# Performance work log

Measured on AMD Instinct MI355X. Metric: run time of the kernel, lower is better.

Reference implementation:

```python
import jax, jax.numpy as jnp
import numpy as np


def squash(v, axis=-1):
    # scale = |v|^2 / (1+|v|^2) / |v|  (exactly as in the source)
    s2 = jnp.sum(jnp.square(v), axis=axis, keepdims=True)
    scale = s2 / (1.0 + s2) / jnp.sqrt(s2)
    return scale * v


def setup_inputs() -> dict:
    key = jax.random.key(0)
    k1, k2 = jax.random.split(key)
    B, I, P = 64, 2048, 16   # batch, input_num_capsule, input_dim_vector
    J, D = 32, 32            # num_capsule, dim_vector
    inputs = jax.random.normal(k1, (B, I, P), dtype=jnp.float32)
    W = jax.random.normal(k2, (I, J, P, D), dtype=jnp.float32) * 0.1
    bias = jnp.zeros((1, I, J, 1, 1), dtype=jnp.float32)
    return {"inputs": inputs, "W": W, "bias": bias}


def reference(inputs, W, bias):
    # inputs_hat[b,i,j,d] = inputs[b,i,:] @ W[i,j,:,:]
    # (replaces the tf.scan over batch of per-capsule batch_dot)
    inputs_hat = jnp.einsum('bip,ijpd->bijd', inputs, W)

    # In the source while_loop, c = softmax(self.bias, dim=2) is computed from the
    # ORIGINAL bias every iteration (loop-carried b is never read), so all
    # num_routing iterations yield the identical output; compute it once.
    c = jax.nn.softmax(bias[:, :, :, 0, 0], axis=2)          # [1, I, J]
    s = jnp.einsum('bijd,xij->bjd', inputs_hat, c)            # sum over input capsules
    outputs = squash(s, axis=-1)                              # [B, J, D]
    return outputs
```

## Files before the change

### kernel.cpp

```cpp
#include <hip/hip_runtime.h>
#include <hip/hip_bf16.h>
#include <math.h>

#define I_CAP 2048
#define P_DIM 16
#define J_CAP 32
#define D_DIM 32
#define B_SZ  64
#define KCN   32
#define IPB   (I_CAP / KCN)
#define IPW   (IPB / 4)

typedef __attribute__((ext_vector_type(8)))  short short8_t;
typedef __attribute__((ext_vector_type(16))) float f32x16;

__device__ __forceinline__ short f2bf(float f) {
    __hip_bfloat16 h = __float2bfloat16(f);
    return __builtin_bit_cast(short, h);
}

__global__ __launch_bounds__(256, 2) void caps_main_k(const float* __restrict__ inputs,
                                                      const float* __restrict__ W,
                                                      const float* __restrict__ bias,
                                                      float* __restrict__ partial) {
    __shared__ float red[4 * 4096];
    __shared__ float c_lds[64][2];
    const int t  = threadIdx.x;
    const int l  = t & 63;
    const int wv = t >> 6;

    const int orig = blockIdx.x;
    const int wgid = (orig & 7) * 64 + (orig >> 3);
    const int kc = wgid >> 4;
    const int jp = wgid & 15;
    const int j0 = jp * 2;

    const int g  = l >> 5;
    const int dn = l & 31;

    const int i0blk = kc * IPB;
    const int i0    = i0blk + wv * IPW;

    {
        const int jj = t & 31;
        const int ib = t >> 5;
#pragma unroll
        for (int pass = 0; pass < 8; ++pass) {
            const int ii = pass * 8 + ib;
            float x = bias[(i0blk + ii) * J_CAP + jj];
            float m = x;
#pragma unroll
            for (int k = 16; k >= 1; k >>= 1) m = fmaxf(m, __shfl_xor(m, k));
            float e = expf(x - m);
            float s = e;
#pragma unroll
            for (int k = 16; k >= 1; k >>= 1) s += __shfl_xor(s, k);
            float cv = e / s;
            if (jj == j0)     c_lds[ii][0] = cv;
            if (jj == j0 + 1) c_lds[ii][1] = cv;
        }
    }
    __syncthreads();

    const float* wlane  = W + (((size_t)(i0 * J_CAP + j0)) << 9) + g * 256 + dn;
    const float* alane0 = inputs + ((size_t)dn << 15) + (size_t)i0 * 16 + g * 8;
    const float* alane1 = alane0 + ((size_t)32 << 15);

    f32x16 accA0 = {};
    f32x16 accA1 = {};
    f32x16 accB0 = {};
    f32x16 accB1 = {};

#pragma unroll 4
    for (int r = 0; r < IPW; ++r) {
        const float cj0 = c_lds[wv * IPW + r][0];
        const float cj1 = c_lds[wv * IPW + r][1];
        float w0buf[8], w1buf[8];
#pragma unroll
        for (int e = 0; e < 8; ++e) {
            w0buf[e] = wlane[(size_t)r * 16384 + e * 32];
            w1buf[e] = wlane[(size_t)r * 16384 + 512 + e * 32];
        }
        float4 a0 = *(const float4*)(alane0 + r * 16);
        float4 a1 = *(const float4*)(alane0 + r * 16 + 4);
        float4 a2 = *(const float4*)(alane1 + r * 16);
        float4 a3 = *(const float4*)(alane1 + r * 16 + 4);

        short8_t bf0, bf1, af0, af1;
#pragma unroll
        for (int e = 0; e < 8; ++e) bf0[e] = f2bf(w0buf[e] * cj0);
#pragma unroll
        for (int e = 0; e < 8; ++e) bf1[e] = f2bf(w1buf[e] * cj1);
        af0[0] = f2bf(a0.x); af0[1] = f2bf(a0.y); af0[2] = f2bf(a0.z); af0[3] = f2bf(a0.w);
        af0[4] = f2bf(a1.x); af0[5] = f2bf(a1.y); af0[6] = f2bf(a1.z); af0[7] = f2bf(a1.w);
        af1[0] = f2bf(a2.x); af1[1] = f2bf(a2.y); af1[2] = f2bf(a2.z); af1[3] = f2bf(a2.w);
        af1[4] = f2bf(a3.x); af1[5] = f2bf(a3.y); af1[6] = f2bf(a3.z); af1[7] = f2bf(a3.w);

        accA0 = __builtin_amdgcn_mfma_f32_32x32x16_bf16(af0, bf0, accA0, 0, 0, 0);
        accA1 = __builtin_amdgcn_mfma_f32_32x32x16_bf16(af1, bf0, accA1, 0, 0, 0);
        accB0 = __builtin_amdgcn_mfma_f32_32x32x16_bf16(af0, bf1, accB0, 0, 0, 0);
        accB1 = __builtin_amdgcn_mfma_f32_32x32x16_bf16(af1, bf1, accB1, 0, 0, 0);
    }

    {
        float* rw = red + wv * 4096;
#pragma unroll
        for (int reg = 0; reg < 16; ++reg) {
            const int b0 = (reg & 3) + 8 * (reg >> 2) + 4 * g;
            rw[b0 * 32 + dn]               = accA0[reg];
            rw[(b0 + 32) * 32 + dn]        = accA1[reg];
            rw[2048 + b0 * 32 + dn]        = accB0[reg];
            rw[2048 + (b0 + 32) * 32 + dn] = accB1[reg];
        }
    }
    __syncthreads();
    {
        float* dstbase = partial + (size_t)(kc * J_CAP + j0) * 2048;
#pragma unroll
        for (int jj = 0; jj < 2; ++jj) {
#pragma unroll
            for (int s = 0; s < 2; ++s) {
                const int o = jj * 2048 + s * 1024 + t * 4;
                float4 v0 = *(const float4*)(red + o);
                float4 v1 = *(const float4*)(red + 4096 + o);
                float4 v2 = *(const float4*)(red + 8192 + o);
                float4 v3 = *(const float4*)(red + 12288 + o);
                float4 sum = {v0.x + v1.x + v2.x + v3.x,
                              v0.y + v1.y + v2.y + v3.y,
                              v0.z + v1.z + v2.z + v3.z,
                              v0.w + v1.w + v2.w + v3.w};
                *(float4*)(dstbase + o) = sum;
            }
        }
    }
}

__global__ __launch_bounds__(256) void caps_reduce_squash_k(const float* __restrict__ partial,
                                                            float* __restrict__ out) {
    const int tid2 = blockIdx.x * 256 + threadIdx.x;
    const int row  = tid2 >> 4;
    const int sub  = tid2 & 15;
    const int d4   = sub >> 1;
    const int half = sub & 1;
    const int j = row >> 6, b = row & 63;

    const float* src = partial + ((size_t)(half * 16) * J_CAP + j) * 2048 + b * 32 + d4 * 4;
    float4 v = {0.f, 0.f, 0.f, 0.f};
#pragma unroll
    for (int kc = 0; kc < 16; ++kc) {
        float4 p = *(const float4*)(src + (size_t)kc * J_CAP * 2048);
        v.x += p.x; v.y += p.y; v.z += p.z; v.w += p.w;
    }
    v.x += __shfl_xor(v.x, 1); v.y += __shfl_xor(v.y, 1);
    v.z += __shfl_xor(v.z, 1); v.w += __shfl_xor(v.w, 1);

    float sq = v.x * v.x + v.y * v.y + v.z * v.z + v.w * v.w;
#pragma unroll
    for (int m = 2; m <= 8; m <<= 1) sq += __shfl_xor(sq, m);
    float scale = sq / (1.0f + sq) / sqrtf(sq);
    if (half == 0) {
        float4 o = {v.x * scale, v.y * scale, v.z * scale, v.w * scale};
        *(float4*)(out + (size_t)b * (J_CAP * D_DIM) + j * D_DIM + d4 * 4) = o;
    }
}

extern "C" void kernel_launch(void* const* d_in, const int* in_sizes, int n_in,
                              void* d_out, int out_size, void* d_ws, size_t ws_size,
                              hipStream_t stream) {
    const float* inputs = (const float*)d_in[0];
    const float* W      = (const float*)d_in[1];
    const float* bias   = (const float*)d_in[2];
    float* out = (float*)d_out;

    float* partial = (float*)d_ws;

    caps_main_k<<<dim3(KCN * 16), dim3(256), 0, stream>>>(inputs, W, bias, partial);
    caps_reduce_squash_k<<<dim3(128), dim3(256), 0, stream>>>(partial, out);
}
```

Measured before the change: 39.92 us.

## Widen blocks to 4 output capsules and 8 waves per workgroup

```diff
diff --git a/kernel.cpp b/kernel.cpp
--- a/kernel.cpp
+++ b/kernel.cpp
@@ -9,7 +9,8 @@
 #define B_SZ  64
 #define KCN   32
 #define IPB   (I_CAP / KCN)
-#define IPW   (IPB / 4)
+#define NWAVE 8
+#define IPW   (IPB / NWAVE)
 
 typedef __attribute__((ext_vector_type(8)))  short short8_t;
 typedef __attribute__((ext_vector_type(16))) float f32x16;
@@ -19,21 +20,21 @@
     return __builtin_bit_cast(short, h);
 }
 
-__global__ __launch_bounds__(256, 2) void caps_main_k(const float* __restrict__ inputs,
+__global__ __launch_bounds__(512, 2) void caps_main_k(const float* __restrict__ inputs,
                                                       const float* __restrict__ W,
                                                       const float* __restrict__ bias,
                                                       float* __restrict__ partial) {
-    __shared__ float red[4 * 4096];
-    __shared__ float c_lds[64][2];
+    __shared__ float red[NWAVE * 2048];
+    __shared__ float c_lds[IPB][4];
     const int t  = threadIdx.x;
     const int l  = t & 63;
     const int wv = t >> 6;
 
     const int orig = blockIdx.x;
-    const int wgid = (orig & 7) * 64 + (orig >> 3);
-    const int kc = wgid >> 4;
-    const int jp = wgid & 15;
-    const int j0 = jp * 2;
+    const int wgid = (orig & 7) * 32 + (orig >> 3);
+    const int kc = wgid >> 3;
+    const int jq = wgid & 7;
+    const int j0 = jq * 4;
 
     const int g  = l >> 5;
     const int dn = l & 31;
@@ -44,9 +45,10 @@
     {
         const int jj = t & 31;
         const int ib = t >> 5;
+        const int jr = jj - j0;
 #pragma unroll
-        for (int pass = 0; pass < 8; ++pass) {
-            const int ii = pass * 8 + ib;
+        for (int pass = 0; pass < 4; ++pass) {
+            const int ii = pass * 16 + ib;
             float x = bias[(i0blk + ii) * J_CAP + jj];
             float m = x;
 #pragma unroll
@@ -55,9 +57,7 @@
             float s = e;
 #pragma unroll
             for (int k = 16; k >= 1; k >>= 1) s += __shfl_xor(s, k);
-            float cv = e / s;
-            if (jj == j0)     c_lds[ii][0] = cv;
-            if (jj == j0 + 1) c_lds[ii][1] = cv;
+            if ((unsigned)jr < 4u) c_lds[ii][jr] = e / s;
         }
     }
     __syncthreads();
@@ -66,71 +66,63 @@
     const float* alane0 = inputs + ((size_t)dn << 15) + (size_t)i0 * 16 + g * 8;
     const float* alane1 = alane0 + ((size_t)32 << 15);
 
-    f32x16 accA0 = {};
-    f32x16 accA1 = {};
-    f32x16 accB0 = {};
-    f32x16 accB1 = {};
+    f32x16 acc[4][2];
+#pragma unroll
+    for (int jj = 0; jj < 4; ++jj) { acc[jj][0] = (f32x16){}; acc[jj][1] = (f32x16){}; }
 
-#pragma unroll 4
+#pragma unroll 2
     for (int r = 0; r < IPW; ++r) {
-        const float cj0 = c_lds[wv * IPW + r][0];
-        const float cj1 = c_lds[wv * IPW + r][1];
-        float w0buf[8], w1buf[8];
+        float wb[4][8];
 #pragma unroll
-        for (int e = 0; e < 8; ++e) {
-            w0buf[e] = wlane[(size_t)r * 16384 + e * 32];
-            w1buf[e] = wlane[(size_t)r * 16384 + 512 + e * 32];
-        }
+        for (int jj = 0; jj < 4; ++jj)
+#pragma unroll
+            for (int e = 0; e < 8; ++e)
+                wb[jj][e] = wlane[(size_t)r * 16384 + jj * 512 + e * 32];
+
         float4 a0 = *(const float4*)(alane0 + r * 16);
         float4 a1 = *(const float4*)(alane0 + r * 16 + 4);
         float4 a2 = *(const float4*)(alane1 + r * 16);
         float4 a3 = *(const float4*)(alane1 + r * 16 + 4);
 
-        short8_t bf0, bf1, af0, af1;
-#pragma unroll
-        for (int e = 0; e < 8; ++e) bf0[e] = f2bf(w0buf[e] * cj0);
-#pragma unroll
-        for (int e = 0; e < 8; ++e) bf1[e] = f2bf(w1buf[e] * cj1);
+        short8_t af0, af1;
         af0[0] = f2bf(a0.x); af0[1] = f2bf(a0.y); af0[2] = f2bf(a0.z); af0[3] = f2bf(a0.w);
         af0[4] = f2bf(a1.x); af0[5] = f2bf(a1.y); af0[6] = f2bf(a1.z); af0[7] = f2bf(a1.w);
         af1[0] = f2bf(a2.x); af1[1] = f2bf(a2.y); af1[2] = f2bf(a2.z); af1[3] = f2bf(a2.w);
         af1[4] = f2bf(a3.x); af1[5] = f2bf(a3.y); af1[6] = f2bf(a3.z); af1[7] = f2bf(a3.w);
 
-        accA0 = __builtin_amdgcn_mfma_f32_32x32x16_bf16(af0, bf0, accA0, 0, 0, 0);
-        accA1 = __builtin_amdgcn_mfma_f32_32x32x16_bf16(af1, bf0, accA1, 0, 0, 0);
-        accB0 = __builtin_amdgcn_mfma_f32_32x32x16_bf16(af0, bf1, accB0, 0, 0, 0);
-        accB1 = __builtin_amdgcn_mfma_f32_32x32x16_bf16(af1, bf1, accB1, 0, 0, 0);
+#pragma unroll
+        for (int jj = 0; jj < 4; ++jj) {
+            const float cj = c_lds[wv * IPW + r][jj];
+            short8_t bf;
+#pragma unroll
+            for (int e = 0; e < 8; ++e) bf[e] = f2bf(wb[jj][e] * cj);
+            acc[jj][0] = __builtin_amdgcn_mfma_f32_32x32x16_bf16(af0, bf, acc[jj][0], 0, 0, 0);
+            acc[jj][1] = __builtin_amdgcn_mfma_f32_32x32x16_bf16(af1, bf, acc[jj][1], 0, 0, 0);
+        }
     }
 
-    {
-        float* rw = red + wv * 4096;
 #pragma unroll
-        for (int reg = 0; reg < 16; ++reg) {
-            const int b0 = (reg & 3) + 8 * (reg >> 2) + 4 * g;
-            rw[b0 * 32 + dn]               = accA0[reg];
-            rw[(b0 + 32) * 32 + dn]        = accA1[reg];
-            rw[2048 + b0 * 32 + dn]        = accB0[reg];
-            rw[2048 + (b0 + 32) * 32 + dn] = accB1[reg];
+    for (int jj = 0; jj < 4; ++jj) {
+        __syncthreads();
+        {
+            float* rw = red + wv * 2048;
+#pragma unroll
+            for (int reg = 0; reg < 16; ++reg) {
+                const int b0 = (reg & 3) + 8 * (reg >> 2) + 4 * g;
+                rw[b0 * 32 + dn]        = acc[jj][0][reg];
+                rw[(b0 + 32) * 32 + dn] = acc[jj][1][reg];
+            }
         }
-    }
-    __syncthreads();
-    {
-        float* dstbase = partial + (size_t)(kc * J_CAP + j0) * 2048;
+        __syncthreads();
+        {
+            const int o = t * 4;
+            float4 v = {0.f, 0.f, 0.f, 0.f};
 #pragma unroll
-        for (int jj = 0; jj < 2; ++jj) {
-#pragma unroll
-            for (int s = 0; s < 2; ++s) {
-                const int o = jj * 2048 + s * 1024 + t * 4;
-                float4 v0 = *(const float4*)(red + o);
-                float4 v1 = *(const float4*)(red + 4096 + o);
-                float4 v2 = *(const float4*)(red + 8192 + o);
-                float4 v3 = *(const float4*)(red + 12288 + o);
-                float4 sum = {v0.x + v1.x + v2.x + v3.x,
-                              v0.y + v1.y + v2.y + v3.y,
-                              v0.z + v1.z + v2.z + v3.z,
-                              v0.w + v1.w + v2.w + v3.w};
-                *(float4*)(dstbase + o) = sum;
+            for (int w8 = 0; w8 < NWAVE; ++w8) {
+                float4 p = *(const float4*)(red + w8 * 2048 + o);
+                v.x += p.x; v.y += p.y; v.z += p.z; v.w += p.w;
             }
+            *(float4*)(partial + (size_t)(kc * J_CAP + j0 + jj) * 2048 + o) = v;
         }
     }
 }
@@ -174,6 +166,6 @@
 
     float* partial = (float*)d_ws;
 
-    caps_main_k<<<dim3(KCN * 16), dim3(256), 0, stream>>>(inputs, W, bias, partial);
+    caps_main_k<<<dim3(KCN * 8), dim3(512), 0, stream>>>(inputs, W, bias, partial);
     caps_reduce_squash_k<<<dim3(128), dim3(256), 0, stream>>>(partial, out);
 }
```

New measurement: 35.37 us, median of 2. 11.4% less time.
